# Optimization experiments

Measured on AMD Instinct MI355X. Metric: run time of the kernel, lower is better.

## Reference

```python
import jax, jax.numpy as jnp
import numpy as np

HUMAN_EXHALATION_FLOW = 0.0052  # ENV_CONFIG.HUMAN_EXHALATION_FLOW
TIME_STEP = 1.0                 # ENV_CONFIG.TIME_STEP
N_NODES = 100_000
N_EDGES = 3_200_000
IN_DIM, OUT_DIM, K = 4, 1, 3
T_HIST = 16


def setup_inputs() -> dict:
    key = jax.random.key(0)
    k1, k2, k3, k4, k5 = jax.random.split(key, 5)
    # columns at [:, -1, :]: 0=concentration, 1=people, 2=size (size divides -> keep away from 0)
    origin_data = jax.random.uniform(k1, (N_NODES, T_HIST, 3), jnp.float32, 0.5, 1.5)
    # raw flow field: conv with kernel K (VALID) maps [E+K-1, K, IN_DIM] -> [E, 1, OUT_DIM]
    flow = jax.random.normal(k2, (N_EDGES + K - 1, K, IN_DIM), jnp.float32)
    edge_index = jax.random.randint(k3, (2, N_EDGES), 0, N_NODES, jnp.int32)
    conv_w = jax.random.normal(k4, (OUT_DIM, IN_DIM, K, K), jnp.float32) * 0.1
    conv_b = jax.random.normal(k5, (OUT_DIM,), jnp.float32) * 0.1
    return {"origin_data": origin_data, "flow": flow, "conv_w": conv_w,
            "conv_b": conv_b, "edge_index": edge_index}


def _flow_conv(flow, conv_w, conv_b):
    # [H, W, C] -> [1, C, H, W] -> conv -> [H', W', out_dim]
    x = jnp.transpose(flow, (2, 0, 1))[None]
    y = jax.lax.conv_general_dilated(
        x, conv_w, window_strides=(1, 1), padding='VALID',
        dimension_numbers=('NCHW', 'OIHW', 'NCHW'))
    y = y + conv_b[None, :, None, None]
    return jnp.transpose(y[0], (1, 2, 0))  # [E, 1, out_dim]


def reference(origin_data, flow, conv_w, conv_b, edge_index):
    concentration = origin_data[:, -1, 0]  # [N]
    people = origin_data[:, -1, 1]         # [N]
    size = origin_data[:, -1, 2]           # [N]
    n = concentration.shape[0]
    mask = jnp.ones((n,), concentration.dtype).at[-1].set(0.0)

    fc = _flow_conv(flow, conv_w, conv_b)  # [E, 1, 1]
    val = fc[:, 0, 0]                      # [E]

    src, dst = edge_index[0], edge_index[1]
    # original loop uses .item() everywhere -> these terms are detached from autodiff
    c_sg = jax.lax.stop_gradient(concentration)
    s_sg = jax.lax.stop_gradient(size)
    v_sg = jax.lax.stop_gradient(val)
    msg = jnp.where(src != dst, v_sg * c_sg[src], 0.0)  # skip self-loops
    node_new = jnp.zeros((n,), concentration.dtype)
    node_new = node_new.at[src].add(-msg / s_sg[src] * TIME_STEP)
    node_new = node_new.at[dst].add(msg / s_sg[dst] * TIME_STEP)

    exhaled = HUMAN_EXHALATION_FLOW * jax.lax.stop_gradient(people) / s_sg  # .item() loop -> detached
    result = concentration + (node_new + exhaled * TIME_STEP) * mask
    out2 = jnp.concatenate([edge_index.T.astype(val.dtype), fc[:, :, 0]], axis=1)  # [E, 3]
    return result[:, None], out2
```

## Files before the change

kernel.cpp:

```cpp
#include <hip/hip_runtime.h>


#define WSHIFT 13
#define WSIZE  8192
#define PB     16
#define FPS    8192.0f
#define QBIAS  (1 << 20)
#define QCLMP  ((1 << 19) - 1)

__global__ __launch_bounds__(256) void prep(
    const float* __restrict__ od,
    float* __restrict__ conc,
    unsigned long long* __restrict__ acc,
    int n_nodes)
{
    int n = blockIdx.x * blockDim.x + threadIdx.x;
    if (n >= n_nodes) return;
    conc[n] = od[(long long)n * 48 + 45];
    acc[n]  = 0ULL;
}

__global__ __launch_bounds__(256) void edge_conv(
    const float* __restrict__ flow, const int* __restrict__ ei,
    const float* __restrict__ conv_w, const float* __restrict__ conv_b,
    float* __restrict__ out2, int n_edges)
{
    __shared__ float w[40];
    int t = threadIdx.x;
    if (t < 36) {
        int i  = t & 3;
        int kw = (t >> 2) % 3;
        int kh = t / 12;
        w[t] = conv_w[i * 9 + kh * 3 + kw];
    }
    if (t == 36) w[36] = conv_b[0];
    __syncthreads();

    int e = blockIdx.x * blockDim.x + t;
    if (e >= n_edges) return;

    const float4* fp = (const float4*)(flow + (long long)e * 12);
    float acc = w[36];
#pragma unroll
    for (int q = 0; q < 9; ++q) {
        float4 v = fp[q];
        acc = fmaf(v.x, w[q * 4 + 0], acc);
        acc = fmaf(v.y, w[q * 4 + 1], acc);
        acc = fmaf(v.z, w[q * 4 + 2], acc);
        acc = fmaf(v.w, w[q * 4 + 3], acc);
    }

    float* o = out2 + (long long)e * 3;
    o[0] = (float)ei[e];
    o[1] = (float)ei[n_edges + e];
    o[2] = acc;
}

__global__ __launch_bounds__(1024) void accum(
    const float* __restrict__ out2,
    const float* __restrict__ conc,
    unsigned long long* __restrict__ acc,
    int n_edges, int n_nodes)
{
    __shared__ float tA[WSIZE];
    __shared__ float tB[WSIZE];

    const int w    = blockIdx.x / PB;
    const int sl   = blockIdx.x % PB;
    const int base = w << WSHIFT;

    for (int i = threadIdx.x; i < WSIZE; i += 1024) { tA[i] = 0.f; tB[i] = 0.f; }
    __syncthreads();

    const long long e0 = (long long)sl * n_edges / PB;
    const long long e1 = (long long)(sl + 1) * n_edges / PB;
    for (long long e = e0 + threadIdx.x; e < e1; e += 1024) {
        const float* r = out2 + e * 3;
        float fs = r[0], fd = r[1], v = r[2];
        int s = (int)fs, d = (int)fd;
        if (s == d) continue;
        if ((s >> WSHIFT) == w) atomicAdd(&tA[s - base], v);
        if ((d >> WSHIFT) == w) atomicAdd(&tB[d - base], v * conc[s]);
    }
    __syncthreads();

    for (int i = threadIdx.x; i < WSIZE; i += 1024) {
        int n = base + i;
        if (n >= n_nodes) continue;
        float a = tA[i], b = tB[i];
        if (a == 0.f && b == 0.f) continue;
        int qa = __float2int_rn(a * FPS);
        int qb = __float2int_rn(b * FPS);
        qa = min(max(qa, -QCLMP), QCLMP);
        qb = min(max(qb, -QCLMP), QCLMP);
        unsigned long long enc =
            ((unsigned long long)(unsigned)(qa + QBIAS) << 37) +
            ((unsigned long long)(unsigned)(qb + QBIAS) << 10) + 1ULL;
        atomicAdd(acc + n, enc);
    }
}

__global__ __launch_bounds__(256) void node_final(
    const float* __restrict__ od,
    const float* __restrict__ conc,
    const unsigned long long* __restrict__ acc,
    float* __restrict__ out, int n_nodes)
{
    int n = blockIdx.x * blockDim.x + threadIdx.x;
    if (n >= n_nodes) return;

    unsigned long long t = acc[n];
    long long cnt = (long long)(t & 1023ULL);
    unsigned long long t2 = t >> 10;
    long long sbr = (long long)(t2 & ((1ULL << 27) - 1));
    long long sar = (long long)(t2 >> 27);
    float a = (float)(sar - cnt * QBIAS) * (1.0f / FPS);
    float b = (float)(sbr - cnt * QBIAS) * (1.0f / FPS);

    long long bi = (long long)n * 48 + 45;
    float c  = conc[n];
    float p  = od[bi + 1];
    float is = 1.0f / od[bi + 2];

    float r = c;
    if (n != n_nodes - 1)
        r += (b - a * c) * is + 0.0052f * p * is;
    out[n] = r;
}

extern "C" void kernel_launch(void* const* d_in, const int* in_sizes, int n_in,
                              void* d_out, int out_size, void* d_ws, size_t ws_size,
                              hipStream_t stream) {
    const float* od   = (const float*)d_in[0];
    const float* flow = (const float*)d_in[1];
    const float* cw   = (const float*)d_in[2];
    const float* cb   = (const float*)d_in[3];
    const int*   ei   = (const int*)d_in[4];

    const int n_nodes = in_sizes[0] / 48;
    const int n_edges = in_sizes[4] / 2;

    float* out_res = (float*)d_out;
    float* out2    = out_res + n_nodes;

    float* conc = (float*)d_ws;
    unsigned long long* acc =
        (unsigned long long*)((char*)d_ws + ((size_t)n_nodes * 4 + 7) / 8 * 8);

    const int n_win = (n_nodes + WSIZE - 1) >> WSHIFT;

    dim3 blk(256);
    dim3 grid_nodes((n_nodes + 255) / 256);
    dim3 grid_edges((n_edges + 255) / 256);

    prep<<<grid_nodes, blk, 0, stream>>>(od, conc, acc, n_nodes);
    edge_conv<<<grid_edges, blk, 0, stream>>>(flow, ei, cw, cb, out2, n_edges);
    accum<<<dim3(n_win * PB), dim3(1024), 0, stream>>>(out2, conc, acc,
                                                       n_edges, n_nodes);
    node_final<<<grid_nodes, blk, 0, stream>>>(od, conc, acc, out_res, n_nodes);
}
```

Baseline: 364.9 us.

## Precompute v*conc[src] per edge and replace packed atomics with per-slice partial buffers

The edge_conv kernel now also gathers conc[src] and writes v*conc per edge to a workspace array, so the accumulation kernel no longer does random gathers. The accumulation switches to 16K-node windows with 32 edge slices, blocks mapped across XCDs, and 4-way unrolled loads. Each block writes its window's partial sums with plain stores into per-slice buffers instead of global 64-bit quantized atomics, and the final kernel reduces the 32 slices per node. This adds an extra E-sized write/read and larger partial buffers. It falls back to the old path when the workspace is too small.

```diff
diff --git a/kernel.cpp b/kernel.cpp
--- a/kernel.cpp
+++ b/kernel.cpp
@@ -1,12 +1,16 @@
 #include <hip/hip_runtime.h>
 
 
-#define WSHIFT 13
-#define WSIZE  8192
-#define PB     16
-#define FPS    8192.0f
-#define QBIAS  (1 << 20)
-#define QCLMP  ((1 << 19) - 1)
+#define WSH  14
+#define WSZ  16384
+#define PBF  32
+
+#define OWSH 13
+#define OWSZ 8192
+#define OPB  16
+#define OFPS 8192.0f
+#define OQBIAS (1 << 20)
+#define OQCLMP ((1 << 19) - 1)
 
 __global__ __launch_bounds__(256) void prep(
     const float* __restrict__ od,
@@ -17,13 +21,14 @@
     int n = blockIdx.x * blockDim.x + threadIdx.x;
     if (n >= n_nodes) return;
     conc[n] = od[(long long)n * 48 + 45];
-    acc[n]  = 0ULL;
+    if (acc) acc[n] = 0ULL;
 }
 
 __global__ __launch_bounds__(256) void edge_conv(
     const float* __restrict__ flow, const int* __restrict__ ei,
     const float* __restrict__ conv_w, const float* __restrict__ conv_b,
-    float* __restrict__ out2, int n_edges)
+    const float* __restrict__ conc,
+    float* __restrict__ out2, float* __restrict__ bcv, int n_edges)
 {
     __shared__ float w[40];
     int t = threadIdx.x;
@@ -38,6 +43,10 @@
 
     int e = blockIdx.x * blockDim.x + t;
     if (e >= n_edges) return;
+
+    int s = ei[e];
+    int d = ei[n_edges + e];
+    float cs = bcv ? conc[s] : 0.0f;
 
     const float4* fp = (const float4*)(flow + (long long)e * 12);
     float acc = w[36];
@@ -51,56 +60,157 @@
     }
 
     float* o = out2 + (long long)e * 3;
-    o[0] = (float)ei[e];
-    o[1] = (float)ei[n_edges + e];
+    o[0] = (float)s;
+    o[1] = (float)d;
     o[2] = acc;
-}
-
-__global__ __launch_bounds__(1024) void accum(
+    if (bcv) bcv[e] = acc * cs;
+}
+
+__global__ __launch_bounds__(1024) void accum_f(
+    const float* __restrict__ out2,
+    const float* __restrict__ bcv,
+    float* __restrict__ pA,
+    float* __restrict__ pB,
+    int n_edges, int n_win, int stride)
+{
+    __shared__ float tA[WSZ];
+    __shared__ float tB[WSZ];
+
+    const int xcd = blockIdx.x & 7;
+    const int i   = blockIdx.x >> 3;
+    const int j   = i / n_win;
+    const int sl  = xcd * (PBF >> 3) + j;
+    const int w   = i - j * n_win;
+
+    const int t = threadIdx.x;
+    for (int k = t; k < WSZ; k += 1024) { tA[k] = 0.f; tB[k] = 0.f; }
+    __syncthreads();
+
+    const long long e0 = (long long)sl * n_edges / PBF;
+    const long long e1 = (long long)(sl + 1) * n_edges / PBF;
+
+#define PROC(fs, fd, vv, bb)                                          \
+    {                                                                  \
+        int s_ = (int)(fs), d_ = (int)(fd);                            \
+        if (s_ != d_) {                                                \
+            if ((s_ >> WSH) == w) atomicAdd(&tA[s_ & (WSZ - 1)], (vv));\
+            if ((d_ >> WSH) == w) atomicAdd(&tB[d_ & (WSZ - 1)], (bb));\
+        }                                                              \
+    }
+
+    long long e = e0 + t;
+    for (; e + 3 * 1024 < e1; e += 4 * 1024) {
+        const float* r  = out2 + e * 3;
+        const float* bb = bcv + e;
+        float fs0 = r[0],    fd0 = r[1],    v0 = r[2];
+        float fs1 = r[3072], fd1 = r[3073], v1 = r[3074];
+        float fs2 = r[6144], fd2 = r[6145], v2 = r[6146];
+        float fs3 = r[9216], fd3 = r[9217], v3 = r[9218];
+        float b0 = bb[0], b1 = bb[1024], b2 = bb[2048], b3 = bb[3072];
+        PROC(fs0, fd0, v0, b0);
+        PROC(fs1, fd1, v1, b1);
+        PROC(fs2, fd2, v2, b2);
+        PROC(fs3, fd3, v3, b3);
+    }
+    for (; e < e1; e += 1024) {
+        const float* r = out2 + e * 3;
+        float fs = r[0], fd = r[1], vv = r[2];
+        float bb = bcv[e];
+        PROC(fs, fd, vv, bb);
+    }
+#undef PROC
+    __syncthreads();
+
+    float* dA = pA + (long long)sl * stride + ((long long)w << WSH);
+    float* dB = pB + (long long)sl * stride + ((long long)w << WSH);
+    for (int k = t; k < (WSZ >> 2); k += 1024) {
+        ((float4*)dA)[k] = ((const float4*)tA)[k];
+        ((float4*)dB)[k] = ((const float4*)tB)[k];
+    }
+}
+
+__global__ __launch_bounds__(256) void node_final_f(
+    const float* __restrict__ od,
+    const float* __restrict__ conc,
+    const float* __restrict__ pA,
+    const float* __restrict__ pB,
+    float* __restrict__ out, int n_nodes, int stride)
+{
+    int n = blockIdx.x * blockDim.x + threadIdx.x;
+    if (n >= n_nodes) return;
+
+    float a0 = 0.f, a1 = 0.f, a2 = 0.f, a3 = 0.f;
+    float b0 = 0.f, b1 = 0.f, b2 = 0.f, b3 = 0.f;
+#pragma unroll
+    for (int sl = 0; sl < PBF; sl += 4) {
+        a0 += pA[(long long)(sl + 0) * stride + n];
+        a1 += pA[(long long)(sl + 1) * stride + n];
+        a2 += pA[(long long)(sl + 2) * stride + n];
+        a3 += pA[(long long)(sl + 3) * stride + n];
+        b0 += pB[(long long)(sl + 0) * stride + n];
+        b1 += pB[(long long)(sl + 1) * stride + n];
+        b2 += pB[(long long)(sl + 2) * stride + n];
+        b3 += pB[(long long)(sl + 3) * stride + n];
+    }
+    float a = (a0 + a1) + (a2 + a3);
+    float b = (b0 + b1) + (b2 + b3);
+
+    long long bi = (long long)n * 48 + 45;
+    float c  = conc[n];
+    float p  = od[bi + 1];
+    float is = 1.0f / od[bi + 2];
+
+    float r = c;
+    if (n != n_nodes - 1)
+        r += (b - a * c) * is + 0.0052f * p * is;
+    out[n] = r;
+}
+
+__global__ __launch_bounds__(1024) void accum_o(
     const float* __restrict__ out2,
     const float* __restrict__ conc,
     unsigned long long* __restrict__ acc,
     int n_edges, int n_nodes)
 {
-    __shared__ float tA[WSIZE];
-    __shared__ float tB[WSIZE];
-
-    const int w    = blockIdx.x / PB;
-    const int sl   = blockIdx.x % PB;
-    const int base = w << WSHIFT;
-
-    for (int i = threadIdx.x; i < WSIZE; i += 1024) { tA[i] = 0.f; tB[i] = 0.f; }
-    __syncthreads();
-
-    const long long e0 = (long long)sl * n_edges / PB;
-    const long long e1 = (long long)(sl + 1) * n_edges / PB;
+    __shared__ float tA[OWSZ];
+    __shared__ float tB[OWSZ];
+
+    const int w    = blockIdx.x / OPB;
+    const int sl   = blockIdx.x % OPB;
+    const int base = w << OWSH;
+
+    for (int i = threadIdx.x; i < OWSZ; i += 1024) { tA[i] = 0.f; tB[i] = 0.f; }
+    __syncthreads();
+
+    const long long e0 = (long long)sl * n_edges / OPB;
+    const long long e1 = (long long)(sl + 1) * n_edges / OPB;
     for (long long e = e0 + threadIdx.x; e < e1; e += 1024) {
         const float* r = out2 + e * 3;
         float fs = r[0], fd = r[1], v = r[2];
         int s = (int)fs, d = (int)fd;
         if (s == d) continue;
-        if ((s >> WSHIFT) == w) atomicAdd(&tA[s - base], v);
-        if ((d >> WSHIFT) == w) atomicAdd(&tB[d - base], v * conc[s]);
-    }
-    __syncthreads();
-
-    for (int i = threadIdx.x; i < WSIZE; i += 1024) {
+        if ((s >> OWSH) == w) atomicAdd(&tA[s - base], v);
+        if ((d >> OWSH) == w) atomicAdd(&tB[d - base], v * conc[s]);
+    }
+    __syncthreads();
+
+    for (int i = threadIdx.x; i < OWSZ; i += 1024) {
         int n = base + i;
         if (n >= n_nodes) continue;
         float a = tA[i], b = tB[i];
         if (a == 0.f && b == 0.f) continue;
-        int qa = __float2int_rn(a * FPS);
-        int qb = __float2int_rn(b * FPS);
-        qa = min(max(qa, -QCLMP), QCLMP);
-        qb = min(max(qb, -QCLMP), QCLMP);
+        int qa = __float2int_rn(a * OFPS);
+        int qb = __float2int_rn(b * OFPS);
+        qa = min(max(qa, -OQCLMP), OQCLMP);
+        qb = min(max(qb, -OQCLMP), OQCLMP);
         unsigned long long enc =
-            ((unsigned long long)(unsigned)(qa + QBIAS) << 37) +
-            ((unsigned long long)(unsigned)(qb + QBIAS) << 10) + 1ULL;
+            ((unsigned long long)(unsigned)(qa + OQBIAS) << 37) +
+            ((unsigned long long)(unsigned)(qb + OQBIAS) << 10) + 1ULL;
         atomicAdd(acc + n, enc);
     }
 }
 
-__global__ __launch_bounds__(256) void node_final(
+__global__ __launch_bounds__(256) void node_final_o(
     const float* __restrict__ od,
     const float* __restrict__ conc,
     const unsigned long long* __restrict__ acc,
@@ -114,8 +224,8 @@
     unsigned long long t2 = t >> 10;
     long long sbr = (long long)(t2 & ((1ULL << 27) - 1));
     long long sar = (long long)(t2 >> 27);
-    float a = (float)(sar - cnt * QBIAS) * (1.0f / FPS);
-    float b = (float)(sbr - cnt * QBIAS) * (1.0f / FPS);
+    float a = (float)(sar - cnt * OQBIAS) * (1.0f / OFPS);
+    float b = (float)(sbr - cnt * OQBIAS) * (1.0f / OFPS);
 
     long long bi = (long long)n * 48 + 45;
     float c  = conc[n];
@@ -143,19 +253,44 @@
     float* out_res = (float*)d_out;
     float* out2    = out_res + n_nodes;
 
-    float* conc = (float*)d_ws;
-    unsigned long long* acc =
-        (unsigned long long*)((char*)d_ws + ((size_t)n_nodes * 4 + 7) / 8 * 8);
-
-    const int n_win = (n_nodes + WSIZE - 1) >> WSHIFT;
-
     dim3 blk(256);
     dim3 grid_nodes((n_nodes + 255) / 256);
     dim3 grid_edges((n_edges + 255) / 256);
 
-    prep<<<grid_nodes, blk, 0, stream>>>(od, conc, acc, n_nodes);
-    edge_conv<<<grid_edges, blk, 0, stream>>>(flow, ei, cw, cb, out2, n_edges);
-    accum<<<dim3(n_win * PB), dim3(1024), 0, stream>>>(out2, conc, acc,
-                                                       n_edges, n_nodes);
-    node_final<<<grid_nodes, blk, 0, stream>>>(od, conc, acc, out_res, n_nodes);
-}
+    const int n_win  = (n_nodes + WSZ - 1) >> WSH;
+    const int stride = n_win << WSH;
+    size_t off = 0;
+    size_t o_conc = off; off += (((size_t)n_nodes * 4) + 255) & ~255ULL;
+    size_t o_bc   = off; off += (((size_t)n_edges * 4) + 255) & ~255ULL;
+    size_t o_pA   = off; off += (((size_t)PBF * stride * 4) + 255) & ~255ULL;
+    size_t o_pB   = off; off += (((size_t)PBF * stride * 4) + 255) & ~255ULL;
+    const bool full = (ws_size >= off);
+
+    float* conc = (float*)((char*)d_ws + o_conc);
+
+    if (full) {
+        float* bcv = (float*)((char*)d_ws + o_bc);
+        float* pA  = (float*)((char*)d_ws + o_pA);
+        float* pB  = (float*)((char*)d_ws + o_pB);
+
+        prep<<<grid_nodes, blk, 0, stream>>>(od, conc, nullptr, n_nodes);
+        edge_conv<<<grid_edges, blk, 0, stream>>>(flow, ei, cw, cb, conc,
+                                                  out2, bcv, n_edges);
+        accum_f<<<dim3(n_win * PBF), dim3(1024), 0, stream>>>(
+            out2, bcv, pA, pB, n_edges, n_win, stride);
+        node_final_f<<<grid_nodes, blk, 0, stream>>>(od, conc, pA, pB,
+                                                     out_res, n_nodes, stride);
+    } else {
+        unsigned long long* acc =
+            (unsigned long long*)((char*)d_ws + (((size_t)n_nodes * 4 + 7) / 8 * 8));
+        const int n_win_o = (n_nodes + OWSZ - 1) >> OWSH;
+
+        prep<<<grid_nodes, blk, 0, stream>>>(od, conc, acc, n_nodes);
+        edge_conv<<<grid_edges, blk, 0, stream>>>(flow, ei, cw, cb, conc,
+                                                  out2, nullptr, n_edges);
+        accum_o<<<dim3(n_win_o * OPB), dim3(1024), 0, stream>>>(
+            out2, conc, acc, n_edges, n_nodes);
+        node_final_o<<<grid_nodes, blk, 0, stream>>>(od, conc, acc,
+                                                     out_res, n_nodes);
+    }
+}
```

Measured after the change: 326.3 us. 1.12x faster.
